# Kernel tuning notes

Hardware: AMD Instinct MI355X
Metric: run time of the kernel (lower is better)

Reference implementation:

```python
import jax, jax.numpy as jnp
import numpy as np

N = 50000      # nodes
E = 800000     # edges
F_IN = 128     # numInputFeatures
HID = 64       # numHiddenLayerFeatures
C = 40         # numClasses


def setup_inputs() -> dict:
    key = jax.random.key(0)
    ks = jax.random.split(key, 24)
    def nrm(k, shape, s=0.05):
        return jax.random.normal(k, shape, jnp.float32) * s
    return {
        "x": jax.random.normal(ks[0], (N, F_IN), jnp.float32),
        "edge_index": jax.random.randint(ks[1], (2, E), 0, N, jnp.int64),
        "w": jax.random.normal(ks[2], (3,), jnp.float32),  # ensemble weights
        # GCNConv
        "W_gcn": nrm(ks[3], (F_IN, HID)), "b_gcn": jnp.zeros((HID,), jnp.float32),
        # SAGEConv (lin_l on aggregated neighbors w/ bias, lin_r on root no bias)
        "Wl_sage": nrm(ks[4], (F_IN, HID)), "bl_sage": jnp.zeros((HID,), jnp.float32),
        "Wr_sage": nrm(ks[5], (F_IN, HID)),
        # GATConv heads=1
        "W_gat": nrm(ks[6], (F_IN, HID)), "att_src": nrm(ks[7], (HID,)),
        "att_dst": nrm(ks[8], (HID,)), "b_gat": jnp.zeros((HID,), jnp.float32),
        # TransformerConv heads=1 (hidden -> classes)
        "Wq": nrm(ks[9], (HID, C)), "bq": jnp.zeros((C,), jnp.float32),
        "Wk": nrm(ks[10], (HID, C)), "bk": jnp.zeros((C,), jnp.float32),
        "Wv": nrm(ks[11], (HID, C)), "bv": jnp.zeros((C,), jnp.float32),
        "Wskip": nrm(ks[12], (HID, C)), "bskip": jnp.zeros((C,), jnp.float32),
    }


def _segment_softmax(e, seg, num_segments):
    m = jax.ops.segment_max(e, seg, num_segments=num_segments)
    ex = jnp.exp(e - m[seg])
    s = jax.ops.segment_sum(ex, seg, num_segments=num_segments)
    return ex / (s[seg] + 1e-16)


def _gcn(x, src, dst, W, b):
    h = x @ W                                        # [N, HID]
    loop = jnp.arange(N, dtype=src.dtype)
    s = jnp.concatenate([src, loop]); d = jnp.concatenate([dst, loop])
    deg = jax.ops.segment_sum(jnp.ones_like(d, jnp.float32), d, num_segments=N)
    dinv = jnp.where(deg > 0, jax.lax.rsqrt(deg), 0.0)
    norm = dinv[s] * dinv[d]                         # [E+N]
    out = jax.ops.segment_sum(h[s] * norm[:, None], d, num_segments=N)
    return out + b


def _sage(x, src, dst, Wl, bl, Wr):
    cnt = jax.ops.segment_sum(jnp.ones((src.shape[0],), jnp.float32), dst, num_segments=N)
    agg = jax.ops.segment_sum(x[src], dst, num_segments=N) / jnp.maximum(cnt, 1.0)[:, None]
    return agg @ Wl + bl + x @ Wr


def _gat(x, src, dst, W, att_src, att_dst, b):
    h = x @ W                                        # [N, HID]
    loop = jnp.arange(N, dtype=src.dtype)
    s = jnp.concatenate([src, loop]); d = jnp.concatenate([dst, loop])
    a_s = h @ att_src; a_d = h @ att_dst             # [N]
    e = jax.nn.leaky_relu(a_s[s] + a_d[d], 0.2)
    alpha = _segment_softmax(e, d, N)
    out = jax.ops.segment_sum(alpha[:, None] * h[s], d, num_segments=N)
    return out + b


def _transformer(x, src, dst, Wq, bq, Wk, bk, Wv, bv, Wskip, bskip):
    q = x @ Wq + bq; k = x @ Wk + bk; v = x @ Wv + bv  # [N, C]
    score = jnp.sum(q[dst] * k[src], axis=-1) / jnp.sqrt(jnp.float32(C))
    alpha = _segment_softmax(score, dst, N)
    out = jax.ops.segment_sum(alpha[:, None] * v[src], dst, num_segments=N)
    return out + (x @ Wskip + bskip)


def reference(x, edge_index, w, W_gcn, b_gcn, Wl_sage, bl_sage, Wr_sage,
              W_gat, att_src, att_dst, b_gat,
              Wq, bq, Wk, bk, Wv, bv, Wskip, bskip):
    src, dst = edge_index[0], edge_index[1]
    gelu = lambda t: jax.nn.gelu(t, approximate=False)
    ens = gelu(_gcn(x, src, dst, W_gcn, b_gcn)) * w[0]
    ens = ens + gelu(_sage(x, src, dst, Wl_sage, bl_sage, Wr_sage)) * w[1]
    ens = ens + gelu(_gat(x, src, dst, W_gat, att_src, att_dst, b_gat)) * w[2]
    out = _transformer(ens, src, dst, Wq, bq, Wk, bk, Wv, bv, Wskip, bskip)
    return jax.nn.log_softmax(out, axis=1)
```

## Files before the change

kernel.cpp:

```cpp
#include <hip/hip_runtime.h>
#include <math.h>

#define NN 50000
#define EE 800000
#define FIN 128
#define HID 64
#define CL 40
#define SCB 256
#define NBLK ((NN + SCB - 1) / SCB)
#define NREP 8
#define QW 256

typedef unsigned short ushort_t;
typedef unsigned int uint_t;
typedef float f32x4 __attribute__((ext_vector_type(4)));
typedef short s16x8 __attribute__((ext_vector_type(8)));

__device__ __forceinline__ ushort_t f2bf(float f) {
  uint_t u = __float_as_uint(f);
  u = (u + 0x7FFFu + ((u >> 16) & 1u)) >> 16;
  return (ushort_t)u;
}
__device__ __forceinline__ uint_t f2bf2(float lo, float hi) {
  return (uint_t)f2bf(lo) | ((uint_t)f2bf(hi) << 16);
}
__device__ __forceinline__ float bf2f(ushort_t s) {
  return __uint_as_float(((uint_t)s) << 16);
}
__device__ __forceinline__ float bflo(uint_t u) {
  return __uint_as_float(u << 16);
}
__device__ __forceinline__ float bfhi(uint_t u) {
  return __uint_as_float(u & 0xFFFF0000u);
}

__device__ __forceinline__ int wave_sum_i(int v) {
#pragma unroll
  for (int off = 32; off > 0; off >>= 1) v += __shfl_xor(v, off, 64);
  return v;
}
__device__ __forceinline__ float half_sum(float v) {
#pragma unroll
  for (int off = 16; off > 0; off >>= 1) v += __shfl_xor(v, off, 64);
  return v;
}
__device__ __forceinline__ float half_max(float v) {
#pragma unroll
  for (int off = 16; off > 0; off >>= 1) v = fmaxf(v, __shfl_xor(v, off, 64));
  return v;
}
__device__ __forceinline__ float gelu_exact(float x) {
  return 0.5f * x * (1.0f + erff(x * 0.70710678118654752f));
}
__device__ __forceinline__ float leaky02(float x) {
  return x >= 0.f ? x : 0.2f * x;
}

#define PREP_CAST 6250
#define PREP_W 169
#define PREP_HIST 3125
__global__ __launch_bounds__(256) void k_prep(
    const float* __restrict__ x, const int* __restrict__ dst,
    const float* __restrict__ W0, const float* __restrict__ W1,
    const float* __restrict__ W2, const float* __restrict__ W3,
    const float* __restrict__ Q0, const float* __restrict__ Q1,
    const float* __restrict__ Q2, const float* __restrict__ Q3,
    const float* __restrict__ b0, const float* __restrict__ b1,
    const float* __restrict__ b2, const float* __restrict__ b3,
    ushort_t* __restrict__ xb, ushort_t* __restrict__ WtA,
    ushort_t* __restrict__ WtB, float* __restrict__ bcat,
    int* __restrict__ cntR, int* __restrict__ erank) {
  int b = blockIdx.x, t = threadIdx.x;
  if (b < PREP_CAST) {
    int i = b * 256 + t;
    if (i < NN * FIN / 4) {
      float4 v = ((const float4*)x)[i];
      ushort4 o;
      o.x = f2bf(v.x); o.y = f2bf(v.y); o.z = f2bf(v.z); o.w = f2bf(v.w);
      ((ushort4*)xb)[i] = o;
    }
  } else if (b < PREP_CAST + PREP_W) {
    int idx = (b - PREP_CAST) * 256 + t;
    if (idx < 32768) {
      int m = idx >> 13, r = idx & 8191, c = r >> 7, k = r & 127;
      const float* W = (m == 0) ? W0 : (m == 1) ? W1 : (m == 2) ? W2 : W3;
      WtA[idx] = f2bf(W[k * HID + c]);
    } else if (idx < 43008) {
      int j = idx - 32768;
      int c = j >> 6, k = j & 63;
      int mm = c / CL, cc = c % CL;
      const float* W = (mm == 0) ? Q0 : (mm == 1) ? Q1 : (mm == 2) ? Q2 : Q3;
      WtB[j] = f2bf(W[k * CL + cc]);
    } else if (idx < 43168) {
      int c = idx - 43008;
      int mm = c / CL, cc = c % CL;
      const float* bb = (mm == 0) ? b0 : (mm == 1) ? b1 : (mm == 2) ? b2 : b3;
      bcat[c] = bb[cc];
    }
  } else {
    int hb = b - PREP_CAST - PREP_W;
    int e = hb * 256 + t;
    if (e < EE) {
      int r = hb & (NREP - 1);
      erank[e] = atomicAdd(&cntR[(size_t)r * NN + dst[e]], 1);
    }
  }
}

__global__ __launch_bounds__(256) void k_gemmA(
    const ushort_t* __restrict__ xb, const ushort_t* __restrict__ WtA,
    const float* __restrict__ attS, const float* __restrict__ attD,
    ushort_t* __restrict__ Hb, float* __restrict__ a_s,
    float* __restrict__ a_d) {
  __shared__ __align__(16) ushort_t wlds[2 * 64 * 136];
  const int t = threadIdx.x;
  const int wv = t >> 6, l = t & 63;
  const int lr = l & 15, lg = l >> 4;
  const int rbase = blockIdx.x * 64 + wv * 16;
  int arow = rbase + lr;
  int arowc = arow < NN ? arow : NN - 1;
  const ushort_t* ap = xb + (size_t)arowc * 128 + lg * 8;
  s16x8 af[4];
#pragma unroll
  for (int ks = 0; ks < 4; ++ks) af[ks] = *(const s16x8*)(ap + ks * 32);
  for (int hf = 0; hf < 2; ++hf) {
    if (hf) __syncthreads();
    for (int idx = t; idx < 2 * 64 * 16; idx += 256) {
      int mm = idx >> 10, r2 = idx & 1023, c = r2 >> 4, ch = r2 & 15;
      *(uint4*)&wlds[(mm * 64 + c) * 136 + ch * 8] =
          *(const uint4*)(WtA + (hf * 2 + mm) * 8192 + c * 128 + ch * 8);
    }
    __syncthreads();
    for (int mm = 0; mm < 2; ++mm) {
      int m = hf * 2 + mm;
      f32x4 acc[4] = {};
#pragma unroll
      for (int ks = 0; ks < 4; ++ks) {
#pragma unroll
        for (int n = 0; n < 4; ++n) {
          s16x8 bf = *(const s16x8*)&wlds[(mm * 64 + n * 16 + lr) * 136 +
                                          ks * 32 + lg * 8];
          acc[n] =
              __builtin_amdgcn_mfma_f32_16x16x32_bf16(af[ks], bf, acc[n], 0, 0, 0);
        }
      }
#pragma unroll
      for (int n = 0; n < 4; ++n) {
#pragma unroll
        for (int j = 0; j < 4; ++j) {
          int orow = rbase + lg * 4 + j;
          if (orow < NN)
            Hb[(size_t)orow * 256 + m * 64 + n * 16 + lr] = f2bf(acc[n][j]);
        }
      }
      if (m == 2) {
        float sat[4], dat[4];
#pragma unroll
        for (int n = 0; n < 4; ++n) {
          sat[n] = attS[n * 16 + lr];
          dat[n] = attD[n * 16 + lr];
        }
#pragma unroll
        for (int j = 0; j < 4; ++j) {
          float ps = 0.f, pd = 0.f;
#pragma unroll
          for (int n = 0; n < 4; ++n) {
            ps = fmaf(acc[n][j], sat[n], ps);
            pd = fmaf(acc[n][j], dat[n], pd);
          }
#pragma unroll
          for (int off = 1; off < 16; off <<= 1) {
            ps += __shfl_xor(ps, off, 64);
            pd += __shfl_xor(pd, off, 64);
          }
          int orow = rbase + lg * 4 + j;
          if (lr == 0 && orow < NN) { a_s[orow] = ps; a_d[orow] = pd; }
        }
      }
    }
  }
}

__global__ __launch_bounds__(SCB) void k_bsum(const int* __restrict__ cntR,
                                              int* __restrict__ bsum) {
  __shared__ int wsm[4];
  int i = blockIdx.x * SCB + threadIdx.x;
  int v = 0;
  if (i < NN) {
#pragma unroll
    for (int r = 0; r < NREP; ++r) v += cntR[(size_t)r * NN + i];
  }
  int s = wave_sum_i(v);
  int lane = threadIdx.x & 63, wv = threadIdx.x >> 6;
  if (lane == 0) wsm[wv] = s;
  __syncthreads();
  if (threadIdx.x == 0) bsum[blockIdx.x] = wsm[0] + wsm[1] + wsm[2] + wsm[3];
}

__global__ __launch_bounds__(SCB) void k_scanapply(
    const int* __restrict__ cntR, const int* __restrict__ bsum,
    const float* __restrict__ a_s, const float* __restrict__ a_d,
    int* __restrict__ cnt, int* __restrict__ offs, int* __restrict__ base8,
    float* __restrict__ dinv, float2* __restrict__ auxS,
    float2* __restrict__ auxD) {
  __shared__ int ts[SCB];
  __shared__ int wred[4];
  int b = blockIdx.x, t = threadIdx.x;
  int pv = (t < b) ? bsum[t] : 0;
  int ps = wave_sum_i(pv);
  int lane = t & 63, wv = t >> 6;
  if (lane == 0) wred[wv] = ps;
  int i = b * SCB + t;
  int cr[NREP];
  int v = 0;
  if (i < NN) {
#pragma unroll
    for (int r = 0; r < NREP; ++r) {
      cr[r] = cntR[(size_t)r * NN + i];
      v += cr[r];
    }
  }
  ts[t] = v;
  __syncthreads();
  int prefix = wred[0] + wred[1] + wred[2] + wred[3];
  for (int off = 1; off < SCB; off <<= 1) {
    int u = (t >= off) ? ts[t - off] : 0;
    __syncthreads();
    ts[t] += u;
    __syncthreads();
  }
  if (i < NN) {
    int ex = ts[t] - v + prefix;
    offs[i] = ex;
    cnt[i] = v;
    float dv = rsqrtf((float)v + 1.0f);
    dinv[i] = dv;
    auxS[i] = make_float2(dv, a_s[i]);
    auxD[i] = make_float2(dv, a_d[i]);
    int run = ex;
#pragma unroll
    for (int r = 0; r < NREP; ++r) {
      base8[(size_t)i * NREP + r] = run;
      run += cr[r];
    }
  }
}

__global__ __launch_bounds__(256) void k_sc1(const int* __restrict__ dst,
                                             const int* __restrict__ erank,
                                             const int* __restrict__ base8,
                                             int* __restrict__ esorted) {
  int e = blockIdx.x * blockDim.x + threadIdx.x;
  if (e < EE) {
    int d = dst[e];
    int r = (e >> 8) & (NREP - 1);
    esorted[base8[(size_t)d * NREP + r] + erank[e]] = e;
  }
}

__global__ __launch_bounds__(256) void k_sc2(
    const int* __restrict__ esorted, const int* __restrict__ src,
    const int* __restrict__ dst, const float2* __restrict__ auxS,
    const float2* __restrict__ auxD, int* __restrict__ srcidx,
    int* __restrict__ dsts, float2* __restrict__ edata) {
  int p = blockIdx.x * blockDim.x + threadIdx.x;
  if (p < EE) {
    int e = esorted[p];
    int s = src[e], d = dst[e];
    srcidx[p] = s;
    dsts[p] = d;
    float2 A = auxS[s];
    float2 B = auxD[d];
    float ex = __expf(leaky02(A.y + B.y));
    edata[p] = make_float2(A.x * B.x, ex);
  }
}

__global__ __launch_bounds__(256) void k_agg1(
    const int* __restrict__ srcidx, const int* __restrict__ offs,
    const int* __restrict__ cnt, const ushort_t* __restrict__ Hb,
    const float2* __restrict__ edata, const float* __restrict__ dinv,
    const float* __restrict__ a_s, const float* __restrict__ a_d,
    const float* __restrict__ b_gcn, const float* __restrict__ bl,
    const float* __restrict__ b_gat, const float* __restrict__ w,
    ushort_t* __restrict__ ensb) {
  int node = (blockIdx.x * blockDim.x + threadIdx.x) >> 6;
  int lane = threadIdx.x & 63;
  if (node >= NN) return;
  const int half = lane >> 5;
  const int fl = lane & 31;
  int beg = offs[node];
  int c = cnt[node];
  int end = beg + c;
  float ag0 = 0.f, ag1 = 0.f, as0 = 0.f, as1 = 0.f, aa0 = 0.f, aa1 = 0.f,
        dg = 0.f;
  int p = beg + half;
  for (; p + 6 < end; p += 8) {
    int sA = srcidx[p], sB = srcidx[p + 2], sC = srcidx[p + 4],
        sD = srcidx[p + 6];
    float2 eA = edata[p], eB = edata[p + 2], eC = edata[p + 4],
           eD = edata[p + 6];
    const uint_t* hA = (const uint_t*)(Hb + (size_t)sA * 256);
    const uint_t* hB = (const uint_t*)(Hb + (size_t)sB * 256);
    const uint_t* hC = (const uint_t*)(Hb + (size_t)sC * 256);
    const uint_t* hD = (const uint_t*)(Hb + (size_t)sD * 256);
    uint_t gA = hA[fl], qA = hA[32 + fl], tA = hA[64 + fl];
    uint_t gB = hB[fl], qB = hB[32 + fl], tB = hB[64 + fl];
    uint_t gC = hC[fl], qC = hC[32 + fl], tC = hC[64 + fl];
    uint_t gD = hD[fl], qD = hD[32 + fl], tD = hD[64 + fl];
    ag0 = fmaf(bflo(gA), eA.x, ag0); ag1 = fmaf(bfhi(gA), eA.x, ag1);
    ag0 = fmaf(bflo(gB), eB.x, ag0); ag1 = fmaf(bfhi(gB), eB.x, ag1);
    ag0 = fmaf(bflo(gC), eC.x, ag0); ag1 = fmaf(bfhi(gC), eC.x, ag1);
    ag0 = fmaf(bflo(gD), eD.x, ag0); ag1 = fmaf(bfhi(gD), eD.x, ag1);
    as0 += (bflo(qA) + bflo(qB)) + (bflo(qC) + bflo(qD));
    as1 += (bfhi(qA) + bfhi(qB)) + (bfhi(qC) + bfhi(qD));
    aa0 = fmaf(bflo(tA), eA.y, aa0); aa1 = fmaf(bfhi(tA), eA.y, aa1);
    aa0 = fmaf(bflo(tB), eB.y, aa0); aa1 = fmaf(bfhi(tB), eB.y, aa1);
    aa0 = fmaf(bflo(tC), eC.y, aa0); aa1 = fmaf(bfhi(tC), eC.y, aa1);
    aa0 = fmaf(bflo(tD), eD.y, aa0); aa1 = fmaf(bfhi(tD), eD.y, aa1);
    dg += (eA.y + eB.y) + (eC.y + eD.y);
  }
  for (; p < end; p += 2) {
    int sA = srcidx[p];
    float2 eA = edata[p];
    const uint_t* hA = (const uint_t*)(Hb + (size_t)sA * 256);
    uint_t gA = hA[fl], qA = hA[32 + fl], tA = hA[64 + fl];
    ag0 = fmaf(bflo(gA), eA.x, ag0); ag1 = fmaf(bfhi(gA), eA.x, ag1);
    as0 += bflo(qA);                 as1 += bfhi(qA);
    aa0 = fmaf(bflo(tA), eA.y, aa0); aa1 = fmaf(bfhi(tA), eA.y, aa1);
    dg += eA.y;
  }
  ag0 += __shfl_xor(ag0, 32, 64); ag1 += __shfl_xor(ag1, 32, 64);
  as0 += __shfl_xor(as0, 32, 64); as1 += __shfl_xor(as1, 32, 64);
  aa0 += __shfl_xor(aa0, 32, 64); aa1 += __shfl_xor(aa1, 32, 64);
  dg += __shfl_xor(dg, 32, 64);
  float dd = dinv[node];
  float exl = __expf(leaky02(a_s[node] + a_d[node]));
  const uint_t* hd = (const uint_t*)(Hb + (size_t)node * 256);
  uint_t hg = hd[fl], ht = hd[64 + fl], hr = hd[96 + fl];
  float2 bg = ((const float2*)b_gcn)[fl];
  float2 bs = ((const float2*)bl)[fl];
  float2 ba = ((const float2*)b_gat)[fl];
  float dd2 = dd * dd;
  float cinv = 1.0f / fmaxf((float)c, 1.0f);
  float gdi = 1.0f / (dg + exl + 1e-16f);
  float g0 = ag0 + dd2 * bflo(hg) + bg.x;
  float g1 = ag1 + dd2 * bfhi(hg) + bg.y;
  float s0 = as0 * cinv + bs.x + bflo(hr);
  float s1 = as1 * cinv + bs.y + bfhi(hr);
  float t0 = (aa0 + exl * bflo(ht)) * gdi + ba.x;
  float t1 = (aa1 + exl * bfhi(ht)) * gdi + ba.y;
  float w0 = w[0], w1 = w[1], w2 = w[2];
  float e0 = w0 * gelu_exact(g0) + w1 * gelu_exact(s0) + w2 * gelu_exact(t0);
  float e1 = w0 * gelu_exact(g1) + w1 * gelu_exact(s1) + w2 * gelu_exact(t1);
  if (half == 0) ((uint_t*)ensb)[(size_t)node * 32 + fl] = f2bf2(e0, e1);
}

__global__ __launch_bounds__(256) void k_gemmB(
    const ushort_t* __restrict__ ensb, const ushort_t* __restrict__ WtB,
    const float* __restrict__ bcat, ushort_t* __restrict__ QKVSb) {
  __shared__ __align__(16) ushort_t wb[160 * 72];
  __shared__ float bsh[160];
  const int t = threadIdx.x;
  for (int idx = t; idx < 160 * 8; idx += 256) {
    int c = idx >> 3, ch = idx & 7;
    *(uint4*)&wb[c * 72 + ch * 8] = *(const uint4*)(WtB + c * 64 + ch * 8);
  }
  if (t < 160) bsh[t] = bcat[t];
  __syncthreads();
  const int wv = t >> 6, l = t & 63;
  const int lr = l & 15, lg = l >> 4;
  const int rbase = blockIdx.x * 64 + wv * 16;
  int arow = rbase + lr;
  int arowc = arow < NN ? arow : NN - 1;
  const ushort_t* ap = ensb + (size_t)arowc * 64 + lg * 8;
  f32x4 acc[10] = {};
#pragma unroll
  for (int ks = 0; ks < 2; ++ks) {
    s16x8 af = *(const s16x8*)(ap + ks * 32);
#pragma unroll
    for (int n = 0; n < 10; ++n) {
      s16x8 bf = *(const s16x8*)&wb[(n * 16 + lr) * 72 + ks * 32 + lg * 8];
      acc[n] = __builtin_amdgcn_mfma_f32_16x16x32_bf16(af, bf, acc[n], 0, 0, 0);
    }
  }
#pragma unroll
  for (int n = 0; n < 10; ++n) {
    int col = n * 16 + lr;
    int seg = col / CL;
    int off = seg * 64 + (col - seg * CL);
#pragma unroll
    for (int j = 0; j < 4; ++j) {
      int orow = rbase + lg * 4 + j;
      if (orow < NN)
        QKVSb[(size_t)orow * QW + off] = f2bf(acc[n][j] + bsh[col]);
    }
  }
}

__global__ __launch_bounds__(256) void k_score(
    const int* __restrict__ srcidx, const int* __restrict__ dsts,
    const ushort_t* __restrict__ QKVSb, float* __restrict__ escore) {
  int p = (blockIdx.x * 256 + threadIdx.x) >> 3;
  int l = threadIdx.x & 7;
  if (p >= EE) return;
  int s = srcidx[p], d = dsts[p];
  float part = 0.f;
  if (l < 5) {
    const uint4 qv = *(const uint4*)(QKVSb + (size_t)d * QW + l * 8);
    const uint4 kv = *(const uint4*)(QKVSb + (size_t)s * QW + 64 + l * 8);
    part = bflo(qv.x) * bflo(kv.x);
    part = fmaf(bfhi(qv.x), bfhi(kv.x), part);
    part = fmaf(bflo(qv.y), bflo(kv.y), part);
    part = fmaf(bfhi(qv.y), bfhi(kv.y), part);
    part = fmaf(bflo(qv.z), bflo(kv.z), part);
    part = fmaf(bfhi(qv.z), bfhi(kv.z), part);
    part = fmaf(bflo(qv.w), bflo(kv.w), part);
    part = fmaf(bfhi(qv.w), bfhi(kv.w), part);
  }
  part += __shfl_xor(part, 1, 64);
  part += __shfl_xor(part, 2, 64);
  part += __shfl_xor(part, 4, 64);
  if (l == 0) escore[p] = __expf(part * 0.15811388300841897f);
}

__global__ __launch_bounds__(256) void k_agg2(
    const int* __restrict__ srcidx, const int* __restrict__ offs,
    const int* __restrict__ cnt, const ushort_t* __restrict__ QKVSb,
    const float* __restrict__ escore, float* __restrict__ out) {
  int node = (blockIdx.x * blockDim.x + threadIdx.x) >> 6;
  int lane = threadIdx.x & 63;
  if (node >= NN) return;
  const int half = lane >> 5;
  const int fl = lane & 31;
  const bool valid = fl < 20;
  int beg = offs[node];
  int end = beg + cnt[node];
  float den = 0.f, av0 = 0.f, av1 = 0.f;
  const int VOFF = 64;
  int p = beg + half;
  for (; p + 6 < end; p += 8) {
    int sA = srcidx[p], sB = srcidx[p + 2], sC = srcidx[p + 4],
        sD = srcidx[p + 6];
    float eA = escore[p], eB = escore[p + 2], eC = escore[p + 4],
          eD = escore[p + 6];
    uint_t vA = valid ? ((const uint_t*)QKVSb)[(size_t)sA * 128 + VOFF + fl] : 0u;
    uint_t vB = valid ? ((const uint_t*)QKVSb)[(size_t)sB * 128 + VOFF + fl] : 0u;
    uint_t vC = valid ? ((const uint_t*)QKVSb)[(size_t)sC * 128 + VOFF + fl] : 0u;
    uint_t vD = valid ? ((const uint_t*)QKVSb)[(size_t)sD * 128 + VOFF + fl] : 0u;
    av0 = fmaf(eA, bflo(vA), av0); av1 = fmaf(eA, bfhi(vA), av1);
    av0 = fmaf(eB, bflo(vB), av0); av1 = fmaf(eB, bfhi(vB), av1);
    av0 = fmaf(eC, bflo(vC), av0); av1 = fmaf(eC, bfhi(vC), av1);
    av0 = fmaf(eD, bflo(vD), av0); av1 = fmaf(eD, bfhi(vD), av1);
    den += (eA + eB) + (eC + eD);
  }
  for (; p < end; p += 2) {
    int sA = srcidx[p];
    float eA = escore[p];
    uint_t vA = valid ? ((const uint_t*)QKVSb)[(size_t)sA * 128 + VOFF + fl] : 0u;
    av0 = fmaf(eA, bflo(vA), av0); av1 = fmaf(eA, bfhi(vA), av1);
    den += eA;
  }
  av0 += __shfl_xor(av0, 32, 64);
  av1 += __shfl_xor(av1, 32, 64);
  den += __shfl_xor(den, 32, 64);
  uint_t sk = valid ? ((const uint_t*)QKVSb)[(size_t)node * 128 + 96 + fl] : 0u;
  float di = 1.0f / (den + 1e-16f);
  float o0 = valid ? av0 * di + bflo(sk) : -3.0e38f;
  float o1 = valid ? av1 * di + bfhi(sk) : -3.0e38f;
  float m = half_max(fmaxf(o0, o1));
  float eo = valid ? __expf(o0 - m) + __expf(o1 - m) : 0.f;
  float ls = logf(half_sum(eo));
  if (valid && half == 0) {
    float2 r = make_float2(o0 - m - ls, o1 - m - ls);
    ((float2*)out)[(size_t)node * 20 + fl] = r;
  }
}

extern "C" void kernel_launch(void* const* d_in, const int* in_sizes, int n_in,
                              void* d_out, int out_size, void* d_ws,
                              size_t ws_size, hipStream_t stream) {
  const float* x     = (const float*)d_in[0];
  const int*   ei    = (const int*)d_in[1];
  const float* w     = (const float*)d_in[2];
  const float* W_gcn = (const float*)d_in[3];
  const float* b_gcn = (const float*)d_in[4];
  const float* Wl    = (const float*)d_in[5];
  const float* bl    = (const float*)d_in[6];
  const float* Wr    = (const float*)d_in[7];
  const float* W_gat = (const float*)d_in[8];
  const float* att_s = (const float*)d_in[9];
  const float* att_d = (const float*)d_in[10];
  const float* b_gat = (const float*)d_in[11];
  const float* Wq    = (const float*)d_in[12];
  const float* bq    = (const float*)d_in[13];
  const float* Wk    = (const float*)d_in[14];
  const float* bk    = (const float*)d_in[15];
  const float* Wv    = (const float*)d_in[16];
  const float* bv    = (const float*)d_in[17];
  const float* Wsk   = (const float*)d_in[18];
  const float* bsk   = (const float*)d_in[19];
  float* out = (float*)d_out;
  float* ws  = (float*)d_ws;

  const int* src = ei;
  const int* dst = ei + EE;

  ushort_t* Hb     = (ushort_t*)ws;
  ushort_t* ensb   = (ushort_t*)(ws + (size_t)128 * NN);
  float*    a_s    = ws + (size_t)160 * NN;
  float*    a_d    = ws + (size_t)161 * NN;
  float*    dinv   = ws + (size_t)162 * NN;
  ushort_t* qkvsb  = (ushort_t*)(ws + (size_t)163 * NN);
  ushort_t* xb     = (ushort_t*)(ws + (size_t)291 * NN);
  ushort_t* WtA    = (ushort_t*)(ws + (size_t)355 * NN);
  ushort_t* WtB    = (ushort_t*)(ws + (size_t)355 * NN + 16384);
  float*    bcat   = ws + (size_t)355 * NN + 21504;
  float*    escore = ws + (size_t)355 * NN + 21664;
  float2*   edata  = (float2*)(ws + (size_t)355 * NN + 21664 + EE);
  float2*   auxS   = (float2*)(ws + (size_t)355 * NN + 21664 + 3 * (size_t)EE);
  float2*   auxD   = auxS + NN;
  int*      ibase  = (int*)(ws + (size_t)359 * NN + 21664 + 3 * (size_t)EE);
  int*      cnt    = ibase;
  int*      offs   = ibase + NN;
  int*      srcidx = ibase + 2 * NN;
  int*      dsts   = ibase + 2 * NN + EE;
  int*      erank  = ibase + 2 * NN + 2 * EE;
  int*      esorted= ibase + 2 * NN + 3 * EE;
  int*      bsum   = ibase + 2 * NN + 4 * EE;
  int*      cntR   = ibase + 2 * NN + 4 * EE + 256;
  int*      base8  = cntR + (size_t)NREP * NN;

  hipMemsetAsync(cntR, 0, (size_t)NREP * NN * sizeof(int), stream);

  k_prep<<<PREP_CAST + PREP_W + PREP_HIST, 256, 0, stream>>>(
      x, dst, W_gcn, Wl, W_gat, Wr, Wq, Wk, Wv, Wsk, bq, bk, bv, bsk, xb, WtA,
      WtB, bcat, cntR, erank);

  k_gemmA<<<(NN + 63) / 64, 256, 0, stream>>>(xb, WtA, att_s, att_d, Hb, a_s,
                                              a_d);
  k_bsum<<<NBLK, SCB, 0, stream>>>(cntR, bsum);
  k_scanapply<<<NBLK, SCB, 0, stream>>>(cntR, bsum, a_s, a_d, cnt, offs, base8,
                                        dinv, auxS, auxD);
  k_sc1<<<(EE + 255) / 256, 256, 0, stream>>>(dst, erank, base8, esorted);
  k_sc2<<<(EE + 255) / 256, 256, 0, stream>>>(esorted, src, dst, auxS, auxD,
                                              srcidx, dsts, edata);
  k_agg1<<<(NN + 3) / 4, 256, 0, stream>>>(srcidx, offs, cnt, Hb, edata, dinv,
                                           a_s, a_d, b_gcn, bl, b_gat, w, ensb);
  k_gemmB<<<(NN + 63) / 64, 256, 0, stream>>>(ensb, WtB, bcat, qkvsb);
  k_score<<<(EE * 8 + 255) / 256, 256, 0, stream>>>(srcidx, dsts, qkvsb,
                                                    escore);
  k_agg2<<<(NN + 3) / 4, 256, 0, stream>>>(srcidx, offs, cnt, qkvsb, escore,
                                           out);
}
```

Baseline: 224.5 us.

## Fuse x bf16 cast into gemmA and split root projection out of gathered features

Drops the separate fp32-to-bf16 cast pass over x in the prep kernel; gemmA now reads fp32 x directly and converts it in registers. It also stores the three neighbor-gathered projections in a 192-wide buffer and the root (SAGE lin_r) projection in its own 64-wide buffer, so rows gathered per edge in agg1 are smaller. The aim is to cut a full read/write pass over x and shrink the gather footprint. In exchange, gemmA reads twice the bytes for x, processes one weight matrix per LDS stage with more barriers, and agg1 makes one extra load per node.

```diff
diff --git a/kernel.cpp b/kernel.cpp
--- a/kernel.cpp
+++ b/kernel.cpp
@@ -10,6 +10,7 @@
 #define NBLK ((NN + SCB - 1) / SCB)
 #define NREP 8
 #define QW 256
+#define HGW 192
 
 typedef unsigned short ushort_t;
 typedef unsigned int uint_t;
@@ -56,31 +57,22 @@
   return x >= 0.f ? x : 0.2f * x;
 }
 
-#define PREP_CAST 6250
 #define PREP_W 169
 #define PREP_HIST 3125
 __global__ __launch_bounds__(256) void k_prep(
-    const float* __restrict__ x, const int* __restrict__ dst,
+    const int* __restrict__ dst,
     const float* __restrict__ W0, const float* __restrict__ W1,
     const float* __restrict__ W2, const float* __restrict__ W3,
     const float* __restrict__ Q0, const float* __restrict__ Q1,
     const float* __restrict__ Q2, const float* __restrict__ Q3,
     const float* __restrict__ b0, const float* __restrict__ b1,
     const float* __restrict__ b2, const float* __restrict__ b3,
-    ushort_t* __restrict__ xb, ushort_t* __restrict__ WtA,
-    ushort_t* __restrict__ WtB, float* __restrict__ bcat,
-    int* __restrict__ cntR, int* __restrict__ erank) {
+    ushort_t* __restrict__ WtA, ushort_t* __restrict__ WtB,
+    float* __restrict__ bcat, int* __restrict__ cntR,
+    int* __restrict__ erank) {
   int b = blockIdx.x, t = threadIdx.x;
-  if (b < PREP_CAST) {
-    int i = b * 256 + t;
-    if (i < NN * FIN / 4) {
-      float4 v = ((const float4*)x)[i];
-      ushort4 o;
-      o.x = f2bf(v.x); o.y = f2bf(v.y); o.z = f2bf(v.z); o.w = f2bf(v.w);
-      ((ushort4*)xb)[i] = o;
-    }
-  } else if (b < PREP_CAST + PREP_W) {
-    int idx = (b - PREP_CAST) * 256 + t;
+  if (b < PREP_W) {
+    int idx = b * 256 + t;
     if (idx < 32768) {
       int m = idx >> 13, r = idx & 8191, c = r >> 7, k = r & 127;
       const float* W = (m == 0) ? W0 : (m == 1) ? W1 : (m == 2) ? W2 : W3;
@@ -98,7 +90,7 @@
       bcat[c] = bb[cc];
     }
   } else {
-    int hb = b - PREP_CAST - PREP_W;
+    int hb = b - PREP_W;
     int e = hb * 256 + t;
     if (e < EE) {
       int r = hb & (NREP - 1);
@@ -108,74 +100,83 @@
 }
 
 __global__ __launch_bounds__(256) void k_gemmA(
-    const ushort_t* __restrict__ xb, const ushort_t* __restrict__ WtA,
+    const float* __restrict__ x, const ushort_t* __restrict__ WtA,
     const float* __restrict__ attS, const float* __restrict__ attD,
-    ushort_t* __restrict__ Hb, float* __restrict__ a_s,
-    float* __restrict__ a_d) {
-  __shared__ __align__(16) ushort_t wlds[2 * 64 * 136];
+    ushort_t* __restrict__ Hg, ushort_t* __restrict__ hroot,
+    float* __restrict__ a_s, float* __restrict__ a_d) {
+  __shared__ __align__(16) ushort_t wlds[64 * 136];
   const int t = threadIdx.x;
   const int wv = t >> 6, l = t & 63;
   const int lr = l & 15, lg = l >> 4;
   const int rbase = blockIdx.x * 64 + wv * 16;
   int arow = rbase + lr;
   int arowc = arow < NN ? arow : NN - 1;
-  const ushort_t* ap = xb + (size_t)arowc * 128 + lg * 8;
+  const float* xp = x + (size_t)arowc * 128 + lg * 8;
   s16x8 af[4];
 #pragma unroll
-  for (int ks = 0; ks < 4; ++ks) af[ks] = *(const s16x8*)(ap + ks * 32);
-  for (int hf = 0; hf < 2; ++hf) {
-    if (hf) __syncthreads();
-    for (int idx = t; idx < 2 * 64 * 16; idx += 256) {
-      int mm = idx >> 10, r2 = idx & 1023, c = r2 >> 4, ch = r2 & 15;
-      *(uint4*)&wlds[(mm * 64 + c) * 136 + ch * 8] =
-          *(const uint4*)(WtA + (hf * 2 + mm) * 8192 + c * 128 + ch * 8);
+  for (int ks = 0; ks < 4; ++ks) {
+    float4 v0 = *(const float4*)(xp + ks * 32);
+    float4 v1 = *(const float4*)(xp + ks * 32 + 4);
+    s16x8 a;
+    a[0] = (short)f2bf(v0.x); a[1] = (short)f2bf(v0.y);
+    a[2] = (short)f2bf(v0.z); a[3] = (short)f2bf(v0.w);
+    a[4] = (short)f2bf(v1.x); a[5] = (short)f2bf(v1.y);
+    a[6] = (short)f2bf(v1.z); a[7] = (short)f2bf(v1.w);
+    af[ks] = a;
+  }
+  for (int m = 0; m < 4; ++m) {
+    if (m) __syncthreads();
+    for (int idx = t; idx < 64 * 16; idx += 256) {
+      int c = idx >> 4, ch = idx & 15;
+      *(uint4*)&wlds[c * 136 + ch * 8] =
+          *(const uint4*)(WtA + m * 8192 + c * 128 + ch * 8);
     }
     __syncthreads();
-    for (int mm = 0; mm < 2; ++mm) {
-      int m = hf * 2 + mm;
-      f32x4 acc[4] = {};
-#pragma unroll
-      for (int ks = 0; ks < 4; ++ks) {
-#pragma unroll
-        for (int n = 0; n < 4; ++n) {
-          s16x8 bf = *(const s16x8*)&wlds[(mm * 64 + n * 16 + lr) * 136 +
-                                          ks * 32 + lg * 8];
-          acc[n] =
-              __builtin_amdgcn_mfma_f32_16x16x32_bf16(af[ks], bf, acc[n], 0, 0, 0);
+    f32x4 acc[4] = {};
+#pragma unroll
+    for (int ks = 0; ks < 4; ++ks) {
+#pragma unroll
+      for (int n = 0; n < 4; ++n) {
+        s16x8 bf = *(const s16x8*)&wlds[(n * 16 + lr) * 136 + ks * 32 + lg * 8];
+        acc[n] =
+            __builtin_amdgcn_mfma_f32_16x16x32_bf16(af[ks], bf, acc[n], 0, 0, 0);
+      }
+    }
+#pragma unroll
+    for (int n = 0; n < 4; ++n) {
+#pragma unroll
+      for (int j = 0; j < 4; ++j) {
+        int orow = rbase + lg * 4 + j;
+        if (orow < NN) {
+          if (m < 3)
+            Hg[(size_t)orow * HGW + m * 64 + n * 16 + lr] = f2bf(acc[n][j]);
+          else
+            hroot[(size_t)orow * 64 + n * 16 + lr] = f2bf(acc[n][j]);
         }
       }
+    }
+    if (m == 2) {
+      float sat[4], dat[4];
 #pragma unroll
       for (int n = 0; n < 4; ++n) {
-#pragma unroll
-        for (int j = 0; j < 4; ++j) {
-          int orow = rbase + lg * 4 + j;
-          if (orow < NN)
-            Hb[(size_t)orow * 256 + m * 64 + n * 16 + lr] = f2bf(acc[n][j]);
+        sat[n] = attS[n * 16 + lr];
+        dat[n] = attD[n * 16 + lr];
+      }
+#pragma unroll
+      for (int j = 0; j < 4; ++j) {
+        float ps = 0.f, pd = 0.f;
+#pragma unroll
+        for (int n = 0; n < 4; ++n) {
+          ps = fmaf(acc[n][j], sat[n], ps);
+          pd = fmaf(acc[n][j], dat[n], pd);
         }
-      }
-      if (m == 2) {
-        float sat[4], dat[4];
-#pragma unroll
-        for (int n = 0; n < 4; ++n) {
-          sat[n] = attS[n * 16 + lr];
-          dat[n] = attD[n * 16 + lr];
+#pragma unroll
+        for (int off = 1; off < 16; off <<= 1) {
+          ps += __shfl_xor(ps, off, 64);
+          pd += __shfl_xor(pd, off, 64);
         }
-#pragma unroll
-        for (int j = 0; j < 4; ++j) {
-          float ps = 0.f, pd = 0.f;
-#pragma unroll
-          for (int n = 0; n < 4; ++n) {
-            ps = fmaf(acc[n][j], sat[n], ps);
-            pd = fmaf(acc[n][j], dat[n], pd);
-          }
-#pragma unroll
-          for (int off = 1; off < 16; off <<= 1) {
-            ps += __shfl_xor(ps, off, 64);
-            pd += __shfl_xor(pd, off, 64);
-          }
-          int orow = rbase + lg * 4 + j;
-          if (lr == 0 && orow < NN) { a_s[orow] = ps; a_d[orow] = pd; }
-        }
+        int orow = rbase + lg * 4 + j;
+        if (lr == 0 && orow < NN) { a_s[orow] = ps; a_d[orow] = pd; }
       }
     }
   }
@@ -278,12 +279,12 @@
 
 __global__ __launch_bounds__(256) void k_agg1(
     const int* __restrict__ srcidx, const int* __restrict__ offs,
-    const int* __restrict__ cnt, const ushort_t* __restrict__ Hb,
-    const float2* __restrict__ edata, const float* __restrict__ dinv,
-    const float* __restrict__ a_s, const float* __restrict__ a_d,
-    const float* __restrict__ b_gcn, const float* __restrict__ bl,
-    const float* __restrict__ b_gat, const float* __restrict__ w,
-    ushort_t* __restrict__ ensb) {
+    const int* __restrict__ cnt, const ushort_t* __restrict__ Hg,
+    const ushort_t* __restrict__ hroot, const float2* __restrict__ edata,
+    const float* __restrict__ dinv, const float* __restrict__ a_s,
+    const float* __restrict__ a_d, const float* __restrict__ b_gcn,
+    const float* __restrict__ bl, const float* __restrict__ b_gat,
+    const float* __restrict__ w, ushort_t* __restrict__ ensb) {
   int node = (blockIdx.x * blockDim.x + threadIdx.x) >> 6;
   int lane = threadIdx.x & 63;
   if (node >= NN) return;
@@ -300,10 +301,10 @@
         sD = srcidx[p + 6];
     float2 eA = edata[p], eB = edata[p + 2], eC = edata[p + 4],
            eD = edata[p + 6];
-    const uint_t* hA = (const uint_t*)(Hb + (size_t)sA * 256);
-    const uint_t* hB = (const uint_t*)(Hb + (size_t)sB * 256);
-    const uint_t* hC = (const uint_t*)(Hb + (size_t)sC * 256);
-    const uint_t* hD = (const uint_t*)(Hb + (size_t)sD * 256);
+    const uint_t* hA = (const uint_t*)(Hg + (size_t)sA * HGW);
+    const uint_t* hB = (const uint_t*)(Hg + (size_t)sB * HGW);
+    const uint_t* hC = (const uint_t*)(Hg + (size_t)sC * HGW);
+    const uint_t* hD = (const uint_t*)(Hg + (size_t)sD * HGW);
     uint_t gA = hA[fl], qA = hA[32 + fl], tA = hA[64 + fl];
     uint_t gB = hB[fl], qB = hB[32 + fl], tB = hB[64 + fl];
     uint_t gC = hC[fl], qC = hC[32 + fl], tC = hC[64 + fl];
@@ -323,7 +324,7 @@
   for (; p < end; p += 2) {
     int sA = srcidx[p];
     float2 eA = edata[p];
-    const uint_t* hA = (const uint_t*)(Hb + (size_t)sA * 256);
+    const uint_t* hA = (const uint_t*)(Hg + (size_t)sA * HGW);
     uint_t gA = hA[fl], qA = hA[32 + fl], tA = hA[64 + fl];
     ag0 = fmaf(bflo(gA), eA.x, ag0); ag1 = fmaf(bfhi(gA), eA.x, ag1);
     as0 += bflo(qA);                 as1 += bfhi(qA);
@@ -336,8 +337,9 @@
   dg += __shfl_xor(dg, 32, 64);
   float dd = dinv[node];
   float exl = __expf(leaky02(a_s[node] + a_d[node]));
-  const uint_t* hd = (const uint_t*)(Hb + (size_t)node * 256);
-  uint_t hg = hd[fl], ht = hd[64 + fl], hr = hd[96 + fl];
+  const uint_t* hd = (const uint_t*)(Hg + (size_t)node * HGW);
+  uint_t hg = hd[fl], ht = hd[64 + fl];
+  uint_t hr = ((const uint_t*)hroot)[(size_t)node * 32 + fl];
   float2 bg = ((const float2*)b_gcn)[fl];
   float2 bs = ((const float2*)bl)[fl];
   float2 ba = ((const float2*)b_gat)[fl];
@@ -506,21 +508,21 @@
   const int* src = ei;
   const int* dst = ei + EE;
 
-  ushort_t* Hb     = (ushort_t*)ws;
+  ushort_t* Hg     = (ushort_t*)ws;
+  ushort_t* hroot  = (ushort_t*)(ws + (size_t)96 * NN);
   ushort_t* ensb   = (ushort_t*)(ws + (size_t)128 * NN);
   float*    a_s    = ws + (size_t)160 * NN;
   float*    a_d    = ws + (size_t)161 * NN;
   float*    dinv   = ws + (size_t)162 * NN;
   ushort_t* qkvsb  = (ushort_t*)(ws + (size_t)163 * NN);
-  ushort_t* xb     = (ushort_t*)(ws + (size_t)291 * NN);
-  ushort_t* WtA    = (ushort_t*)(ws + (size_t)355 * NN);
-  ushort_t* WtB    = (ushort_t*)(ws + (size_t)355 * NN + 16384);
-  float*    bcat   = ws + (size_t)355 * NN + 21504;
-  float*    escore = ws + (size_t)355 * NN + 21664;
-  float2*   edata  = (float2*)(ws + (size_t)355 * NN + 21664 + EE);
-  float2*   auxS   = (float2*)(ws + (size_t)355 * NN + 21664 + 3 * (size_t)EE);
+  ushort_t* WtA    = (ushort_t*)(ws + (size_t)291 * NN);
+  ushort_t* WtB    = (ushort_t*)(ws + (size_t)291 * NN + 16384);
+  float*    bcat   = ws + (size_t)291 * NN + 21504;
+  float*    escore = ws + (size_t)291 * NN + 21664;
+  float2*   edata  = (float2*)(ws + (size_t)291 * NN + 21664 + EE);
+  float2*   auxS   = (float2*)(ws + (size_t)291 * NN + 21664 + 3 * (size_t)EE);
   float2*   auxD   = auxS + NN;
-  int*      ibase  = (int*)(ws + (size_t)359 * NN + 21664 + 3 * (size_t)EE);
+  int*      ibase  = (int*)(ws + (size_t)295 * NN + 21664 + 3 * (size_t)EE);
   int*      cnt    = ibase;
   int*      offs   = ibase + NN;
   int*      srcidx = ibase + 2 * NN;
@@ -533,20 +535,21 @@
 
   hipMemsetAsync(cntR, 0, (size_t)NREP * NN * sizeof(int), stream);
 
-  k_prep<<<PREP_CAST + PREP_W + PREP_HIST, 256, 0, stream>>>(
-      x, dst, W_gcn, Wl, W_gat, Wr, Wq, Wk, Wv, Wsk, bq, bk, bv, bsk, xb, WtA,
-      WtB, bcat, cntR, erank);
-
-  k_gemmA<<<(NN + 63) / 64, 256, 0, stream>>>(xb, WtA, att_s, att_d, Hb, a_s,
-                                              a_d);
+  k_prep<<<PREP_W + PREP_HIST, 256, 0, stream>>>(
+      dst, W_gcn, Wl, W_gat, Wr, Wq, Wk, Wv, Wsk, bq, bk, bv, bsk, WtA, WtB,
+      bcat, cntR, erank);
+
+  k_gemmA<<<(NN + 63) / 64, 256, 0, stream>>>(x, WtA, att_s, att_d, Hg, hroot,
+                                              a_s, a_d);
   k_bsum<<<NBLK, SCB, 0, stream>>>(cntR, bsum);
   k_scanapply<<<NBLK, SCB, 0, stream>>>(cntR, bsum, a_s, a_d, cnt, offs, base8,
                                         dinv, auxS, auxD);
   k_sc1<<<(EE + 255) / 256, 256, 0, stream>>>(dst, erank, base8, esorted);
   k_sc2<<<(EE + 255) / 256, 256, 0, stream>>>(esorted, src, dst, auxS, auxD,
                                               srcidx, dsts, edata);
-  k_agg1<<<(NN + 3) / 4, 256, 0, stream>>>(srcidx, offs, cnt, Hb, edata, dinv,
-                                           a_s, a_d, b_gcn, bl, b_gat, w, ensb);
+  k_agg1<<<(NN + 3) / 4, 256, 0, stream>>>(srcidx, offs, cnt, Hg, hroot, edata,
+                                           dinv, a_s, a_d, b_gcn, bl, b_gat, w,
+                                           ensb);
   k_gemmB<<<(NN + 63) / 64, 256, 0, stream>>>(ensb, WtB, bcat, qkvsb);
   k_score<<<(EE * 8 + 255) / 256, 256, 0, stream>>>(srcidx, dsts, qkvsb,
                                                     escore);
```

Measured after the change: 219.3 us. 1.02x faster.
